# Kernel optimization log

Hardware: AMD Instinct MI355X
Metric: run time of the kernel (lower is better)

## Reference

```python
import jax, jax.numpy as jnp
import numpy as np

IN_DIM = 8192
OUT_DIM = 8192
BATCH = 2048


def setup_inputs() -> dict:
    key = jax.random.key(0)
    k1, k2, k3, k4 = jax.random.split(key, 4)
    x = jax.random.uniform(k1, (BATCH, IN_DIM), dtype=jnp.float32)  # soft bits in [0,1]
    weights = jax.random.normal(k2, (OUT_DIM, 16), dtype=jnp.float32)
    idx_a = jax.random.randint(k3, (OUT_DIM,), 0, IN_DIM, dtype=jnp.int64)
    idx_b = jax.random.randint(k4, (OUT_DIM,), 0, IN_DIM, dtype=jnp.int64)
    return {"x": x, "weights": weights, "idx_a": idx_a, "idx_b": idx_b}


def _gate_values(a, b):
    # The 16 real-valued relaxations of the 2-input binary logic gates.
    ab = a * b
    return [
        jnp.zeros_like(a),      # 0:  False
        ab,                     # 1:  a AND b
        a - ab,                 # 2:  a AND NOT b
        a,                      # 3:  a
        b - ab,                 # 4:  NOT a AND b
        b,                      # 5:  b
        a + b - 2.0 * ab,       # 6:  a XOR b
        a + b - ab,             # 7:  a OR b
        1.0 - (a + b - ab),     # 8:  NOT (a OR b)
        1.0 - (a + b - 2.0 * ab),  # 9: NOT (a XOR b)
        1.0 - b,                # 10: NOT b
        1.0 - b + ab,           # 11: a OR NOT b
        1.0 - a,                # 12: NOT a
        1.0 - a + ab,           # 13: NOT a OR b
        1.0 - ab,               # 14: NOT (a AND b)
        jnp.ones_like(a),       # 15: True
    ]


def reference(x, weights, idx_a, idx_b):
    # training=True path of LogicLayer.forward_python
    a = x[:, idx_a]  # [B, OUT]
    b = x[:, idx_b]  # [B, OUT]
    w = jax.nn.softmax(weights, axis=-1)  # [OUT, 16]
    gates = _gate_values(a, b)
    out = jnp.zeros_like(a)
    for k in range(16):  # fixed small structural loop over the 16 gates
        out = out + w[None, :, k] * gates[k]
    return out
```

## Files before the change

### kernel.cpp

```cpp
#include <hip/hip_runtime.h>
#include <hip/hip_fp16.h>

#define IN_DIM 8192
#define OUT_DIM 8192
#define BATCH 2048

#define TPB 512
#define JT 2
#define JTILE (OUT_DIM / JT)
#define OPT (JTILE / TPB / 4)
#define RROWS 4
#define SVEC (IN_DIM / 4 / TPB)

typedef float fvec4 __attribute__((ext_vector_type(4)));

#define BAR_LGKM() __asm__ __volatile__("s_waitcnt lgkmcnt(0)\n\ts_barrier" ::: "memory")

__global__ __launch_bounds__(256) void coeff_kernel(
    const float* __restrict__ w,
    const int* __restrict__ idx_a,
    const int* __restrict__ idx_b,
    int* __restrict__ pidx,
    __half2* __restrict__ pc1,
    __half2* __restrict__ pc2)
{
    int j = blockIdx.x * blockDim.x + threadIdx.x;
    if (j >= OUT_DIM) return;

    const float* wj = w + (size_t)j * 16;
    float wv[16];
    float m = -1e30f;
#pragma unroll
    for (int k = 0; k < 16; ++k) { wv[k] = wj[k]; m = fmaxf(m, wv[k]); }
    float s = 0.f;
#pragma unroll
    for (int k = 0; k < 16; ++k) { wv[k] = __expf(wv[k] - m); s += wv[k]; }
    float inv = 1.0f / s;
#pragma unroll
    for (int k = 0; k < 16; ++k) wv[k] *= inv;

    float c0  = wv[8] + wv[9] + wv[10] + wv[11] + wv[12] + wv[13] + wv[14] + wv[15];
    float ca  = wv[2] + wv[3] + wv[6] + wv[7] - wv[8] - wv[9] - wv[12] - wv[13];
    float cb  = wv[4] + wv[5] + wv[6] + wv[7] - wv[8] - wv[9] - wv[10] - wv[11];
    float cab = wv[1] - wv[2] - wv[4] - 2.f * wv[6] - wv[7]
              + wv[8] + 2.f * wv[9] + wv[11] + wv[13] - wv[14];

    pidx[j] = (idx_a[j] & 0xffff) | (idx_b[j] << 16);
    pc1[j]  = __floats2half2_rn(c0, ca);
    pc2[j]  = __floats2half2_rn(cb, cab);
}

__global__ __launch_bounds__(TPB, 8) void logic_kernel(
    const float* __restrict__ x,
    const int* __restrict__ pidx,
    const __half2* __restrict__ pc1,
    const __half2* __restrict__ pc2,
    float* __restrict__ out)
{
    __shared__ float xrow[IN_DIM];

    const int jt   = blockIdx.x & (JT - 1);
    const int rg   = blockIdx.x / JT;
    const int row0 = rg * RROWS;
    const int jb4  = jt * (JTILE / 4);
    const int tid  = threadIdx.x;

    const int4* pidx4 = (const int4*)pidx;
    const int4* pc14  = (const int4*)pc1;
    const int4* pc24  = (const int4*)pc2;

    int4 pi[OPT], h1[OPT], h2[OPT];
#pragma unroll
    for (int it = 0; it < OPT; ++it) {
        int j4 = jb4 + it * TPB + tid;
        pi[it] = pidx4[j4];
        h1[it] = pc14[j4];
        h2[it] = pc24[j4];
    }

    float4 pf[SVEC];
    {
        const float4* xr4 = (const float4*)(x + (size_t)row0 * IN_DIM);
#pragma unroll
        for (int k = 0; k < SVEC; ++k) pf[k] = xr4[k * TPB + tid];
    }

#pragma unroll
    for (int r = 0; r < RROWS; ++r) {
        BAR_LGKM();

        float4* buf4 = (float4*)xrow;
#pragma unroll
        for (int k = 0; k < SVEC; ++k) buf4[k * TPB + tid] = pf[k];

        if (r + 1 < RROWS) {
            const float4* xr4 = (const float4*)(x + (size_t)(row0 + r + 1) * IN_DIM);
#pragma unroll
            for (int k = 0; k < SVEC; ++k) pf[k] = xr4[k * TPB + tid];
        }

        BAR_LGKM();

        fvec4* out4 = (fvec4*)(out + (size_t)(row0 + r) * OUT_DIM);
#pragma unroll
        for (int it = 0; it < OPT; ++it) {
            int j4 = jb4 + it * TPB + tid;

            int i0 = pi[it].x, i1 = pi[it].y, i2 = pi[it].z, i3 = pi[it].w;
            float a0 = xrow[i0 & 0xffff], b0 = xrow[i0 >> 16];
            float a1 = xrow[i1 & 0xffff], b1 = xrow[i1 >> 16];
            float a2 = xrow[i2 & 0xffff], b2 = xrow[i2 >> 16];
            float a3 = xrow[i3 & 0xffff], b3 = xrow[i3 >> 16];

            float2 f10 = __half22float2(*(const __half2*)&h1[it].x);
            float2 f11 = __half22float2(*(const __half2*)&h1[it].y);
            float2 f12 = __half22float2(*(const __half2*)&h1[it].z);
            float2 f13 = __half22float2(*(const __half2*)&h1[it].w);
            float2 f20 = __half22float2(*(const __half2*)&h2[it].x);
            float2 f21 = __half22float2(*(const __half2*)&h2[it].y);
            float2 f22 = __half22float2(*(const __half2*)&h2[it].z);
            float2 f23 = __half22float2(*(const __half2*)&h2[it].w);

            fvec4 o;
            o.x = f10.x + f10.y * a0 + f20.x * b0 + f20.y * (a0 * b0);
            o.y = f11.x + f11.y * a1 + f21.x * b1 + f21.y * (a1 * b1);
            o.z = f12.x + f12.y * a2 + f22.x * b2 + f22.y * (a2 * b2);
            o.w = f13.x + f13.y * a3 + f23.x * b3 + f23.y * (a3 * b3);
            __builtin_nontemporal_store(o, &out4[j4]);
        }
    }
}

extern "C" void kernel_launch(void* const* d_in, const int* in_sizes, int n_in,
                              void* d_out, int out_size, void* d_ws, size_t ws_size,
                              hipStream_t stream)
{
    const float* x       = (const float*)d_in[0];
    const float* weights = (const float*)d_in[1];
    const int*   idx_a   = (const int*)d_in[2];
    const int*   idx_b   = (const int*)d_in[3];
    float* out = (float*)d_out;

    int*     pidx = (int*)d_ws;
    __half2* pc1  = (__half2*)(pidx + OUT_DIM);
    __half2* pc2  = pc1 + OUT_DIM;

    coeff_kernel<<<OUT_DIM / 256, 256, 0, stream>>>(weights, idx_a, idx_b, pidx, pc1, pc2);
    logic_kernel<<<JT * (BATCH / RROWS), TPB, 0, stream>>>(x, pidx, pc1, pc2, out);
}
```

Before: 147.2 us.

## Process one full batch row per block instead of split-column multi-row tiles

Measured after the change: 141.5 us. 3.9% less time.

```diff
diff --git a/kernel.cpp b/kernel.cpp
--- a/kernel.cpp
+++ b/kernel.cpp
@@ -4,13 +4,8 @@
 #define IN_DIM 8192
 #define OUT_DIM 8192
 #define BATCH 2048
-
 #define TPB 512
-#define JT 2
-#define JTILE (OUT_DIM / JT)
-#define OPT (JTILE / TPB / 4)
-#define RROWS 4
-#define SVEC (IN_DIM / 4 / TPB)
+#define NIT (OUT_DIM / 4 / TPB)
 
 typedef float fvec4 __attribute__((ext_vector_type(4)));
 
@@ -50,6 +45,28 @@
     pc2[j]  = __floats2half2_rn(cb, cab);
 }
 
+#define COMP(IT, PI, H1, H2)                                                   \
+    do {                                                                       \
+        float a0 = xrow[(PI).x & 0xffff], b0 = xrow[(unsigned)(PI).x >> 16];   \
+        float a1 = xrow[(PI).y & 0xffff], b1 = xrow[(unsigned)(PI).y >> 16];   \
+        float a2 = xrow[(PI).z & 0xffff], b2 = xrow[(unsigned)(PI).z >> 16];   \
+        float a3 = xrow[(PI).w & 0xffff], b3 = xrow[(unsigned)(PI).w >> 16];   \
+        float2 f10 = __half22float2(*(const __half2*)&(H1).x);                 \
+        float2 f11 = __half22float2(*(const __half2*)&(H1).y);                 \
+        float2 f12 = __half22float2(*(const __half2*)&(H1).z);                 \
+        float2 f13 = __half22float2(*(const __half2*)&(H1).w);                 \
+        float2 f20 = __half22float2(*(const __half2*)&(H2).x);                 \
+        float2 f21 = __half22float2(*(const __half2*)&(H2).y);                 \
+        float2 f22 = __half22float2(*(const __half2*)&(H2).z);                 \
+        float2 f23 = __half22float2(*(const __half2*)&(H2).w);                 \
+        fvec4 o;                                                               \
+        o.x = f10.x + f10.y * a0 + f20.x * b0 + f20.y * (a0 * b0);             \
+        o.y = f11.x + f11.y * a1 + f21.x * b1 + f21.y * (a1 * b1);             \
+        o.z = f12.x + f12.y * a2 + f22.x * b2 + f22.y * (a2 * b2);             \
+        o.w = f13.x + f13.y * a3 + f23.x * b3 + f23.y * (a3 * b3);             \
+        __builtin_nontemporal_store(o, &out4[(IT) * TPB + tid]);               \
+    } while (0)
+
 __global__ __launch_bounds__(TPB, 8) void logic_kernel(
     const float* __restrict__ x,
     const int* __restrict__ pidx,
@@ -59,76 +76,39 @@
 {
     __shared__ float xrow[IN_DIM];
 
-    const int jt   = blockIdx.x & (JT - 1);
-    const int rg   = blockIdx.x / JT;
-    const int row0 = rg * RROWS;
-    const int jb4  = jt * (JTILE / 4);
-    const int tid  = threadIdx.x;
+    const int row = blockIdx.x;
+    const int tid = threadIdx.x;
+
+    const float4* xr4 = (const float4*)(x + (size_t)row * IN_DIM);
+    float4 pf0 = xr4[tid];
+    float4 pf1 = xr4[TPB + tid];
+    float4 pf2 = xr4[2 * TPB + tid];
+    float4 pf3 = xr4[3 * TPB + tid];
 
     const int4* pidx4 = (const int4*)pidx;
     const int4* pc14  = (const int4*)pc1;
     const int4* pc24  = (const int4*)pc2;
 
-    int4 pi[OPT], h1[OPT], h2[OPT];
-#pragma unroll
-    for (int it = 0; it < OPT; ++it) {
-        int j4 = jb4 + it * TPB + tid;
-        pi[it] = pidx4[j4];
-        h1[it] = pc14[j4];
-        h2[it] = pc24[j4];
-    }
+    int4 pi0 = pidx4[tid],           h10 = pc14[tid],           h20 = pc24[tid];
+    int4 pi1 = pidx4[TPB + tid],     h11 = pc14[TPB + tid],     h21 = pc24[TPB + tid];
 
-    float4 pf[SVEC];
-    {
-        const float4* xr4 = (const float4*)(x + (size_t)row0 * IN_DIM);
-#pragma unroll
-        for (int k = 0; k < SVEC; ++k) pf[k] = xr4[k * TPB + tid];
-    }
+    float4* buf4 = (float4*)xrow;
+    buf4[tid]           = pf0;
+    buf4[TPB + tid]     = pf1;
+    buf4[2 * TPB + tid] = pf2;
+    buf4[3 * TPB + tid] = pf3;
 
-#pragma unroll
-    for (int r = 0; r < RROWS; ++r) {
-        BAR_LGKM();
+    BAR_LGKM();
 
-        float4* buf4 = (float4*)xrow;
-#pragma unroll
-        for (int k = 0; k < SVEC; ++k) buf4[k * TPB + tid] = pf[k];
+    fvec4* out4 = (fvec4*)(out + (size_t)row * OUT_DIM);
 
-        if (r + 1 < RROWS) {
-            const float4* xr4 = (const float4*)(x + (size_t)(row0 + r + 1) * IN_DIM);
-#pragma unroll
-            for (int k = 0; k < SVEC; ++k) pf[k] = xr4[k * TPB + tid];
-        }
+    int4 pi2 = pidx4[2 * TPB + tid], h12 = pc14[2 * TPB + tid], h22 = pc24[2 * TPB + tid];
+    int4 pi3 = pidx4[3 * TPB + tid], h13 = pc14[3 * TPB + tid], h23 = pc24[3 * TPB + tid];
 
-        BAR_LGKM();
-
-        fvec4* out4 = (fvec4*)(out + (size_t)(row0 + r) * OUT_DIM);
-#pragma unroll
-        for (int it = 0; it < OPT; ++it) {
-            int j4 = jb4 + it * TPB + tid;
-
-            int i0 = pi[it].x, i1 = pi[it].y, i2 = pi[it].z, i3 = pi[it].w;
-            float a0 = xrow[i0 & 0xffff], b0 = xrow[i0 >> 16];
-            float a1 = xrow[i1 & 0xffff], b1 = xrow[i1 >> 16];
-            float a2 = xrow[i2 & 0xffff], b2 = xrow[i2 >> 16];
-            float a3 = xrow[i3 & 0xffff], b3 = xrow[i3 >> 16];
-
-            float2 f10 = __half22float2(*(const __half2*)&h1[it].x);
-            float2 f11 = __half22float2(*(const __half2*)&h1[it].y);
-            float2 f12 = __half22float2(*(const __half2*)&h1[it].z);
-            float2 f13 = __half22float2(*(const __half2*)&h1[it].w);
-            float2 f20 = __half22float2(*(const __half2*)&h2[it].x);
-            float2 f21 = __half22float2(*(const __half2*)&h2[it].y);
-            float2 f22 = __half22float2(*(const __half2*)&h2[it].z);
-            float2 f23 = __half22float2(*(const __half2*)&h2[it].w);
-
-            fvec4 o;
-            o.x = f10.x + f10.y * a0 + f20.x * b0 + f20.y * (a0 * b0);
-            o.y = f11.x + f11.y * a1 + f21.x * b1 + f21.y * (a1 * b1);
-            o.z = f12.x + f12.y * a2 + f22.x * b2 + f22.y * (a2 * b2);
-            o.w = f13.x + f13.y * a3 + f23.x * b3 + f23.y * (a3 * b3);
-            __builtin_nontemporal_store(o, &out4[j4]);
-        }
-    }
+    COMP(0, pi0, h10, h20);
+    COMP(1, pi1, h11, h21);
+    COMP(2, pi2, h12, h22);
+    COMP(3, pi3, h13, h23);
 }
 
 extern "C" void kernel_launch(void* const* d_in, const int* in_sizes, int n_in,
@@ -146,5 +126,5 @@
     __half2* pc2  = pc1 + OUT_DIM;
 
     coeff_kernel<<<OUT_DIM / 256, 256, 0, stream>>>(weights, idx_a, idx_b, pidx, pc1, pc2);
-    logic_kernel<<<JT * (BATCH / RROWS), TPB, 0, stream>>>(x, pidx, pc1, pc2, out);
+    logic_kernel<<<BATCH, TPB, 0, stream>>>(x, pidx, pc1, pc2, out);
 }
```
